# Performance work log

Hardware: AMD Instinct MI355X
Metric: run time of the kernel (lower is better)

## Reference

```python
import jax, jax.numpy as jnp
import numpy as np

N = 100000        # num nodes
F_IN = 256        # params['topo_feature']
C = 128           # params['num_edge'] (hidden & GCN channels)
E = 1_600_000     # num edges (avg degree 16)


def setup_inputs() -> dict:
    key = jax.random.key(0)
    k = jax.random.split(key, 6)
    x = jax.random.normal(k[0], (N, F_IN), dtype=jnp.float32)
    edge_index = jax.random.randint(k[1], (2, E), 0, N, dtype=jnp.int32)
    # fc1: Linear(F_IN, C)
    W1 = jax.random.normal(k[2], (C, F_IN), dtype=jnp.float32) * (1.0 / np.sqrt(F_IN))
    b1 = jnp.zeros((C,), dtype=jnp.float32)
    # GCNConv linear: Linear(C, C, bias=False) weight + separate bias added post-aggregation
    W2 = jax.random.normal(k[3], (C, C), dtype=jnp.float32) * (1.0 / np.sqrt(C))
    b2 = jnp.zeros((C,), dtype=jnp.float32)
    return {"x": x, "edge_index": edge_index, "W1": W1, "b1": b1, "W2": W2, "b2": b2}


def reference(x, edge_index, W1, b1, W2, b2):
    # fc1 + relu
    h = jax.nn.relu(x @ W1.T + b1)                       # [N, C]
    # GCNConv: transform, add self-loops, sym-normalize, scatter-add
    z = h @ W2.T                                         # [N, C]
    loop = jnp.arange(N, dtype=edge_index.dtype)
    src = jnp.concatenate([edge_index[0], loop])         # [E+N]
    dst = jnp.concatenate([edge_index[1], loop])         # [E+N]
    deg = jax.ops.segment_sum(jnp.ones_like(dst, jnp.float32), dst, num_segments=N)
    dinv = jnp.where(deg > 0, jax.lax.rsqrt(jnp.maximum(deg, 1.0)), 0.0)
    norm = (dinv[src] * dinv[dst])[:, None]              # [E+N, 1]
    out = jax.ops.segment_sum(z[src] * norm, dst, num_segments=N) + b2
    return out
```

## Files before the change

kernel.cpp:

```cpp
#include <hip/hip_runtime.h>

typedef unsigned short ushort;
typedef __bf16 bf16x8 __attribute__((ext_vector_type(8)));
typedef float f32x4 __attribute__((ext_vector_type(4)));

#define F_IN 256
#define CCH  128
#define BSH  7
#define BNODES 128
#define NBUCK_PAD 1024
#define CHUNK 8192

#define LDA 40
#define EPS 152

__device__ __forceinline__ ushort f2bf(float f) {
    union { float f; unsigned i; } u; u.f = f;
    unsigned r = u.i + 0x7fffu + ((u.i >> 16) & 1u);
    return (ushort)(r >> 16);
}
__device__ __forceinline__ float2 bf2f2(unsigned u) {
    union { unsigned i; float f; } lo, hi;
    lo.i = u << 16;
    hi.i = u & 0xffff0000u;
    return make_float2(lo.f, hi.f);
}

__global__ void cvt_w(const float* __restrict__ w, ushort* __restrict__ wb, int n) {
    int i = blockIdx.x * 256 + threadIdx.x;
    if (i < n) wb[i] = f2bf(w[i]);
}

template<int MODE>
__global__ __launch_bounds__(256)
void gemm_mfma(const void* __restrict__ Ain, const ushort* __restrict__ Wb,
               const float* __restrict__ bias, const float* __restrict__ dinv,
               ushort* __restrict__ Cout, int M, int K)
{
    __shared__ ushort smem[128 * EPS];
    ushort* As = smem;
    ushort* Bs = smem + 128 * LDA;
    const int tid = threadIdx.x;
    const int wave = tid >> 6, lane = tid & 63;
    const int wm = (wave & 1) * 64, wn = (wave >> 1) * 64;
    const int lr = lane & 15;
    const int lq = lane >> 4;
    const int m0 = blockIdx.x * 128;

    f32x4 acc[4][4] = {};

    for (int k0 = 0; k0 < K; k0 += 32) {
        if (MODE == 0) {
            const float* A = (const float*)Ain;
#pragma unroll
            for (int it = 0; it < 2; it++) {
                int flat = tid + it * 256;
                int row = flat >> 2, kq = (flat & 3) * 8;
                float4 a0 = make_float4(0.f, 0.f, 0.f, 0.f);
                float4 a1 = make_float4(0.f, 0.f, 0.f, 0.f);
                if (m0 + row < M) {
                    a0 = *(const float4*)&A[(long)(m0 + row) * K + k0 + kq];
                    a1 = *(const float4*)&A[(long)(m0 + row) * K + k0 + kq + 4];
                }
                ushort u[8] = { f2bf(a0.x), f2bf(a0.y), f2bf(a0.z), f2bf(a0.w),
                                f2bf(a1.x), f2bf(a1.y), f2bf(a1.z), f2bf(a1.w) };
                *(uint4*)&As[row * LDA + kq] = *(uint4*)u;
            }
        } else {
            const ushort* A = (const ushort*)Ain;
#pragma unroll
            for (int it = 0; it < 2; it++) {
                int flat = tid + it * 256;
                int row = flat >> 2, kq = (flat & 3) * 8;
                uint4 a = make_uint4(0u, 0u, 0u, 0u);
                if (m0 + row < M)
                    a = *(const uint4*)&A[(long)(m0 + row) * K + k0 + kq];
                *(uint4*)&As[row * LDA + kq] = a;
            }
        }
#pragma unroll
        for (int it = 0; it < 2; it++) {
            int flat = tid + it * 256;
            int row = flat >> 2, kq = (flat & 3) * 8;
            uint4 b = *(const uint4*)&Wb[(long)row * K + k0 + kq];
            *(uint4*)&Bs[row * LDA + kq] = b;
        }
        __syncthreads();

        bf16x8 af[4], bfr[4];
#pragma unroll
        for (int t4 = 0; t4 < 4; t4++) {
            af[t4]  = *(bf16x8*)&As[(wm + t4 * 16 + lr) * LDA + lq * 8];
            bfr[t4] = *(bf16x8*)&Bs[(wn + t4 * 16 + lr) * LDA + lq * 8];
        }
#pragma unroll
        for (int i = 0; i < 4; i++)
#pragma unroll
            for (int j = 0; j < 4; j++)
                acc[i][j] = __builtin_amdgcn_mfma_f32_16x16x32_bf16(af[i], bfr[j], acc[i][j], 0, 0, 0);
        __syncthreads();
    }

    if (MODE == 0) {
        float bv[4];
#pragma unroll
        for (int j = 0; j < 4; j++) bv[j] = bias[wn + j * 16 + lr];
#pragma unroll
        for (int i = 0; i < 4; i++)
#pragma unroll
            for (int r = 0; r < 4; r++) {
                int row = wm + i * 16 + lq * 4 + r;
#pragma unroll
                for (int j = 0; j < 4; j++) {
                    float v = fmaxf(acc[i][j][r] + bv[j], 0.f);
                    smem[row * EPS + wn + j * 16 + lr] = f2bf(v);
                }
            }
    } else {
#pragma unroll
        for (int i = 0; i < 4; i++)
#pragma unroll
            for (int r = 0; r < 4; r++) {
                int row = wm + i * 16 + lq * 4 + r;
                float di = (m0 + row < M) ? dinv[m0 + row] : 0.f;
#pragma unroll
                for (int j = 0; j < 4; j++)
                    smem[row * EPS + wn + j * 16 + lr] = f2bf(acc[i][j][r] * di);
            }
    }
    __syncthreads();
    {
        int colq = tid & 15, row0 = tid >> 4;
#pragma unroll
        for (int i = 0; i < 8; i++) {
            int row = row0 + i * 16;
            if (m0 + row < M)
                *(uint4*)&Cout[(long)(m0 + row) * CCH + colq * 8] =
                    *(uint4*)&smem[row * EPS + colq * 8];
        }
    }
}

__global__ void zero1024(int* g) { g[threadIdx.x] = 0; }

__global__ __launch_bounds__(256)
void hist_kernel(const int* __restrict__ dst, int* __restrict__ ghist, int E)
{
    __shared__ int h[NBUCK_PAD];
    int t = threadIdx.x;
    for (int i = t; i < NBUCK_PAD; i += 256) h[i] = 0;
    __syncthreads();
    int cb = blockIdx.x * CHUNK;
    int ce = min(cb + CHUNK, E);
    for (int e = cb + t; e < ce; e += 256)
        atomicAdd(&h[dst[e] >> BSH], 1);
    __syncthreads();
    for (int i = t; i < NBUCK_PAD; i += 256)
        if (h[i]) atomicAdd(&ghist[i], h[i]);
}

__global__ void scan1024(const int* __restrict__ ghist, int* __restrict__ base,
                         int* __restrict__ cursor)
{
    __shared__ int s[NBUCK_PAD];
    int t = threadIdx.x;
    int v = ghist[t];
    s[t] = v;
    __syncthreads();
    for (int off = 1; off < 1024; off <<= 1) {
        int x = (t >= off) ? s[t - off] : 0;
        __syncthreads();
        s[t] += x;
        __syncthreads();
    }
    int excl = s[t] - v;
    base[t] = excl;
    cursor[t] = excl;
    if (t == 1023) base[1024] = s[t];
}

__global__ __launch_bounds__(256)
void partition_kernel(const int* __restrict__ src, const int* __restrict__ dst,
                      int* __restrict__ cursor, unsigned* __restrict__ pairs, int E)
{
    __shared__ int lhist[NBUCK_PAD];
    __shared__ int lbase[NBUCK_PAD];
    __shared__ int rbase[NBUCK_PAD];
    __shared__ int ssum[256];
    __shared__ uint2 staged[CHUNK];
    int t = threadIdx.x;
    for (int i = t; i < NBUCK_PAD; i += 256) lhist[i] = 0;
    __syncthreads();
    int cb = blockIdx.x * CHUNK;
    int ce = min(cb + CHUNK, E);
    for (int e = cb + t; e < ce; e += 256)
        atomicAdd(&lhist[dst[e] >> BSH], 1);
    __syncthreads();
    int a0 = lhist[4 * t], a1 = lhist[4 * t + 1], a2 = lhist[4 * t + 2], a3 = lhist[4 * t + 3];
    int tsum = a0 + a1 + a2 + a3;
    ssum[t] = tsum;
    __syncthreads();
    for (int off = 1; off < 256; off <<= 1) {
        int x = (t >= off) ? ssum[t - off] : 0;
        __syncthreads();
        ssum[t] += x;
        __syncthreads();
    }
    int texcl = ssum[t] - tsum;
    lbase[4 * t]     = texcl;
    lbase[4 * t + 1] = texcl + a0;
    lbase[4 * t + 2] = texcl + a0 + a1;
    lbase[4 * t + 3] = texcl + a0 + a1 + a2;
    for (int i = t; i < NBUCK_PAD; i += 256) {
        int c = lhist[i];
        rbase[i] = c ? atomicAdd(&cursor[i], c) : 0;
        lhist[i] = 0;
    }
    __syncthreads();
    for (int e = cb + t; e < ce; e += 256) {
        int d = dst[e];
        int b = d >> BSH;
        unsigned packed = ((unsigned)src[e] << BSH) | (unsigned)(d & (BNODES - 1));
        int p = lbase[b] + atomicAdd(&lhist[b], 1);
        staged[p] = make_uint2(packed, (unsigned)b);
    }
    __syncthreads();
    int cnt = ce - cb;
    for (int i = t; i < cnt; i += 256) {
        uint2 sp = staged[i];
        int b = (int)sp.y;
        pairs[rbase[b] + (i - lbase[b])] = sp.x;
    }
}

__global__ __launch_bounds__(256)
void bucket_csr(const unsigned* __restrict__ pairs, const int* __restrict__ base,
                int* __restrict__ row_start, float* __restrict__ dinv,
                unsigned* __restrict__ csr, int N, int E)
{
    __shared__ int deg[BNODES];
    __shared__ int s[BNODES];
    __shared__ int cur[BNODES];
    const int b = blockIdx.x, t = threadIdx.x;
    if (t < BNODES) deg[t] = 0;
    __syncthreads();
    const int rb = base[b], re = base[b + 1];
    for (int e = rb + t; e < re; e += 256)
        atomicAdd(&deg[pairs[e] & (BNODES - 1)], 1);
    __syncthreads();
    int v = (t < BNODES) ? deg[t] : 0;
    if (t < BNODES) s[t] = v;
    __syncthreads();
    for (int off = 1; off < BNODES; off <<= 1) {
        int x = (t >= off && t < BNODES) ? s[t - off] : 0;
        __syncthreads();
        if (t < BNODES) s[t] += x;
        __syncthreads();
    }
    const int n0 = b << BSH;
    if (t < BNODES) {
        int excl = s[t] - v;
        cur[t] = excl;
        if (n0 + t < N) {
            row_start[n0 + t] = rb + excl;
            dinv[n0 + t] = rsqrtf((float)v + 1.0f);
        }
    }
    if (b == gridDim.x - 1 && t == 0) row_start[N] = E;
    __syncthreads();
    for (int e = rb + t; e < re; e += 256) {
        unsigned p = pairs[e];
        int l = p & (BNODES - 1);
        int slot = atomicAdd(&cur[l], 1);
        csr[rb + slot] = p >> BSH;
    }
}

__global__ __launch_bounds__(256)
void gather_nodes(const unsigned* __restrict__ zq, const unsigned* __restrict__ csr,
                  const int* __restrict__ row_start, const float* __restrict__ dinv,
                  const float* __restrict__ b2, float* __restrict__ out, int N)
{
    const int node = blockIdx.x * 4 + (threadIdx.x >> 6);
    const int lane = threadIdx.x & 63;
    if (node >= N) return;

    float2 zs = bf2f2(zq[(long)node * 64 + lane]);
    float acc0 = zs.x, acc1 = zs.y;

    const int rs = row_start[node];
    const int re = row_start[node + 1];
    int j = rs;
    for (; j + 8 <= re; j += 8) {
        unsigned sI[8], zv[8];
#pragma unroll
        for (int q = 0; q < 8; q++) sI[q] = csr[j + q];
#pragma unroll
        for (int q = 0; q < 8; q++) zv[q] = zq[(long)sI[q] * 64 + lane];
#pragma unroll
        for (int q = 0; q < 8; q++) { float2 f = bf2f2(zv[q]); acc0 += f.x; acc1 += f.y; }
    }
    for (; j < re; j++) {
        float2 f = bf2f2(zq[(long)csr[j] * 64 + lane]);
        acc0 += f.x; acc1 += f.y;
    }

    float di = dinv[node];
    float2 o;
    o.x = b2[lane * 2 + 0] + di * acc0;
    o.y = b2[lane * 2 + 1] + di * acc1;
    *(float2*)&out[(long)node * CCH + lane * 2] = o;
}

extern "C" void kernel_launch(void* const* d_in, const int* in_sizes, int n_in,
                              void* d_out, int out_size, void* d_ws, size_t ws_size,
                              hipStream_t stream)
{
    const float* x  = (const float*)d_in[0];
    const int*   ei = (const int*)d_in[1];
    const float* W1 = (const float*)d_in[2];
    const float* b1 = (const float*)d_in[3];
    const float* W2 = (const float*)d_in[4];
    const float* b2 = (const float*)d_in[5];
    float* out = (float*)d_out;

    const int N = in_sizes[0] / F_IN;
    const int E = in_sizes[1] / 2;
    const int* src = ei;
    const int* dst = ei + E;

    char* ws = (char*)d_ws;
    ushort* h     = (ushort*)ws;   ws += (size_t)N * CCH * 2;
    ushort* zq    = (ushort*)ws;   ws += (size_t)N * CCH * 2;
    ushort* w1b   = (ushort*)ws;   ws += (size_t)CCH * F_IN * 2;
    ushort* w2b   = (ushort*)ws;   ws += (size_t)CCH * CCH * 2;
    unsigned* prs = (unsigned*)ws; ws += (size_t)E * 4;
    unsigned* csr = (unsigned*)ws; ws += (size_t)E * 4;
    int* rstart   = (int*)ws;      ws += ((size_t)N + 1) * 4;
    float* dinv   = (float*)ws;    ws += (size_t)N * 4;
    int* ghist    = (int*)ws;      ws += NBUCK_PAD * 4;
    int* gbase    = (int*)ws;      ws += (NBUCK_PAD + 1) * 4;
    int* gcursor  = (int*)ws;      ws += NBUCK_PAD * 4;

    const int nchunks = (E + CHUNK - 1) / CHUNK;
    const int nbuck   = (N + BNODES - 1) / BNODES;
    const int ngrid   = (N + 127) / 128;

    zero1024<<<1, 1024, 0, stream>>>(ghist);
    hist_kernel<<<nchunks, 256, 0, stream>>>(dst, ghist, E);
    scan1024<<<1, 1024, 0, stream>>>(ghist, gbase, gcursor);
    partition_kernel<<<nchunks, 256, 0, stream>>>(src, dst, gcursor, prs, E);
    bucket_csr<<<nbuck, 256, 0, stream>>>(prs, gbase, rstart, dinv, csr, N, E);

    cvt_w<<<(CCH * F_IN + 255) / 256, 256, 0, stream>>>(W1, w1b, CCH * F_IN);
    cvt_w<<<(CCH * CCH + 255) / 256, 256, 0, stream>>>(W2, w2b, CCH * CCH);

    gemm_mfma<0><<<ngrid, 256, 0, stream>>>(x, w1b, b1, nullptr, h, N, F_IN);
    gemm_mfma<1><<<ngrid, 256, 0, stream>>>(h, w2b, nullptr, dinv, zq, N, CCH);

    gather_nodes<<<(N + 3) / 4, 256, 0, stream>>>((const unsigned*)zq, csr, rstart, dinv, b2, out, N);
}
```

Baseline: 355.7 us.

## Fuse both GEMMs and make edge partition deterministic via per-chunk histograms

Fuses the fc1 and GCN linear GEMMs into one kernel that keeps the ReLU'd hidden tile in shared memory, so the intermediate h never round-trips through global memory. The edge partition now writes per-chunk histograms, and a 2D scan turns them into fixed offsets. This replaces global atomic cursors and removes the histogram recomputation inside partition. Weight conversion is folded into the histogram kernel launch, which cuts the launch count. The trade-off is a serial per-bucket scan over all chunks in a single block, and more shared memory per GEMM block.

```diff
diff --git a/kernel.cpp b/kernel.cpp
--- a/kernel.cpp
+++ b/kernel.cpp
@@ -8,11 +8,11 @@
 #define CCH  128
 #define BSH  7
 #define BNODES 128
-#define NBUCK_PAD 1024
+#define NBUCK 1024
 #define CHUNK 8192
 
 #define LDA 40
-#define EPS 152
+#define LDH 136
 
 __device__ __forceinline__ ushort f2bf(float f) {
     union { float f; unsigned i; } u; u.f = f;
@@ -26,178 +26,72 @@
     return make_float2(lo.f, hi.f);
 }
 
-__global__ void cvt_w(const float* __restrict__ w, ushort* __restrict__ wb, int n) {
-    int i = blockIdx.x * 256 + threadIdx.x;
-    if (i < n) wb[i] = f2bf(w[i]);
-}
-
-template<int MODE>
-__global__ __launch_bounds__(256)
-void gemm_mfma(const void* __restrict__ Ain, const ushort* __restrict__ Wb,
-               const float* __restrict__ bias, const float* __restrict__ dinv,
-               ushort* __restrict__ Cout, int M, int K)
-{
-    __shared__ ushort smem[128 * EPS];
-    ushort* As = smem;
-    ushort* Bs = smem + 128 * LDA;
-    const int tid = threadIdx.x;
-    const int wave = tid >> 6, lane = tid & 63;
-    const int wm = (wave & 1) * 64, wn = (wave >> 1) * 64;
-    const int lr = lane & 15;
-    const int lq = lane >> 4;
-    const int m0 = blockIdx.x * 128;
-
-    f32x4 acc[4][4] = {};
-
-    for (int k0 = 0; k0 < K; k0 += 32) {
-        if (MODE == 0) {
-            const float* A = (const float*)Ain;
-#pragma unroll
-            for (int it = 0; it < 2; it++) {
-                int flat = tid + it * 256;
-                int row = flat >> 2, kq = (flat & 3) * 8;
-                float4 a0 = make_float4(0.f, 0.f, 0.f, 0.f);
-                float4 a1 = make_float4(0.f, 0.f, 0.f, 0.f);
-                if (m0 + row < M) {
-                    a0 = *(const float4*)&A[(long)(m0 + row) * K + k0 + kq];
-                    a1 = *(const float4*)&A[(long)(m0 + row) * K + k0 + kq + 4];
-                }
-                ushort u[8] = { f2bf(a0.x), f2bf(a0.y), f2bf(a0.z), f2bf(a0.w),
-                                f2bf(a1.x), f2bf(a1.y), f2bf(a1.z), f2bf(a1.w) };
-                *(uint4*)&As[row * LDA + kq] = *(uint4*)u;
-            }
-        } else {
-            const ushort* A = (const ushort*)Ain;
-#pragma unroll
-            for (int it = 0; it < 2; it++) {
-                int flat = tid + it * 256;
-                int row = flat >> 2, kq = (flat & 3) * 8;
-                uint4 a = make_uint4(0u, 0u, 0u, 0u);
-                if (m0 + row < M)
-                    a = *(const uint4*)&A[(long)(m0 + row) * K + k0 + kq];
-                *(uint4*)&As[row * LDA + kq] = a;
-            }
-        }
-#pragma unroll
-        for (int it = 0; it < 2; it++) {
-            int flat = tid + it * 256;
-            int row = flat >> 2, kq = (flat & 3) * 8;
-            uint4 b = *(const uint4*)&Wb[(long)row * K + k0 + kq];
-            *(uint4*)&Bs[row * LDA + kq] = b;
-        }
-        __syncthreads();
-
-        bf16x8 af[4], bfr[4];
-#pragma unroll
-        for (int t4 = 0; t4 < 4; t4++) {
-            af[t4]  = *(bf16x8*)&As[(wm + t4 * 16 + lr) * LDA + lq * 8];
-            bfr[t4] = *(bf16x8*)&Bs[(wn + t4 * 16 + lr) * LDA + lq * 8];
-        }
-#pragma unroll
-        for (int i = 0; i < 4; i++)
-#pragma unroll
-            for (int j = 0; j < 4; j++)
-                acc[i][j] = __builtin_amdgcn_mfma_f32_16x16x32_bf16(af[i], bfr[j], acc[i][j], 0, 0, 0);
-        __syncthreads();
-    }
-
-    if (MODE == 0) {
-        float bv[4];
-#pragma unroll
-        for (int j = 0; j < 4; j++) bv[j] = bias[wn + j * 16 + lr];
-#pragma unroll
-        for (int i = 0; i < 4; i++)
-#pragma unroll
-            for (int r = 0; r < 4; r++) {
-                int row = wm + i * 16 + lq * 4 + r;
-#pragma unroll
-                for (int j = 0; j < 4; j++) {
-                    float v = fmaxf(acc[i][j][r] + bv[j], 0.f);
-                    smem[row * EPS + wn + j * 16 + lr] = f2bf(v);
-                }
-            }
-    } else {
-#pragma unroll
-        for (int i = 0; i < 4; i++)
-#pragma unroll
-            for (int r = 0; r < 4; r++) {
-                int row = wm + i * 16 + lq * 4 + r;
-                float di = (m0 + row < M) ? dinv[m0 + row] : 0.f;
-#pragma unroll
-                for (int j = 0; j < 4; j++)
-                    smem[row * EPS + wn + j * 16 + lr] = f2bf(acc[i][j][r] * di);
-            }
-    }
-    __syncthreads();
-    {
-        int colq = tid & 15, row0 = tid >> 4;
-#pragma unroll
-        for (int i = 0; i < 8; i++) {
-            int row = row0 + i * 16;
-            if (m0 + row < M)
-                *(uint4*)&Cout[(long)(m0 + row) * CCH + colq * 8] =
-                    *(uint4*)&smem[row * EPS + colq * 8];
-        }
-    }
-}
-
-__global__ void zero1024(int* g) { g[threadIdx.x] = 0; }
-
-__global__ __launch_bounds__(256)
-void hist_kernel(const int* __restrict__ dst, int* __restrict__ ghist, int E)
-{
-    __shared__ int h[NBUCK_PAD];
-    int t = threadIdx.x;
-    for (int i = t; i < NBUCK_PAD; i += 256) h[i] = 0;
-    __syncthreads();
-    int cb = blockIdx.x * CHUNK;
-    int ce = min(cb + CHUNK, E);
+__global__ __launch_bounds__(256)
+void hist_cvt(const int* __restrict__ dst, int* __restrict__ hist2D, int E, int nchunks,
+              const float* __restrict__ W1, const float* __restrict__ W2,
+              ushort* __restrict__ w1b, ushort* __restrict__ w2b)
+{
+    const int blk = blockIdx.x, t = threadIdx.x;
+    if (blk >= nchunks) {
+        int i = (blk - nchunks) * 256 + t;
+        if (i < CCH * F_IN) w1b[i] = f2bf(W1[i]);
+        else {
+            int j = i - CCH * F_IN;
+            if (j < CCH * CCH) w2b[j] = f2bf(W2[j]);
+        }
+        return;
+    }
+    __shared__ int h[NBUCK];
+    for (int i = t; i < NBUCK; i += 256) h[i] = 0;
+    __syncthreads();
+    int cb = blk * CHUNK, ce = min(cb + CHUNK, E);
     for (int e = cb + t; e < ce; e += 256)
         atomicAdd(&h[dst[e] >> BSH], 1);
     __syncthreads();
-    for (int i = t; i < NBUCK_PAD; i += 256)
-        if (h[i]) atomicAdd(&ghist[i], h[i]);
-}
-
-__global__ void scan1024(const int* __restrict__ ghist, int* __restrict__ base,
-                         int* __restrict__ cursor)
-{
-    __shared__ int s[NBUCK_PAD];
-    int t = threadIdx.x;
-    int v = ghist[t];
-    s[t] = v;
-    __syncthreads();
-    for (int off = 1; off < 1024; off <<= 1) {
+    for (int i = t; i < NBUCK; i += 256)
+        hist2D[blk * NBUCK + i] = h[i];
+}
+
+__global__ __launch_bounds__(1024)
+void scan2d(const int* __restrict__ hist2D, int* __restrict__ pref2D,
+            int* __restrict__ base, int nchunks)
+{
+    __shared__ int s[NBUCK];
+    const int t = threadIdx.x;
+    int run = 0;
+#pragma unroll 4
+    for (int c = 0; c < nchunks; c++) {
+        int v = hist2D[c * NBUCK + t];
+        pref2D[c * NBUCK + t] = run;
+        run += v;
+    }
+    s[t] = run;
+    __syncthreads();
+    for (int off = 1; off < NBUCK; off <<= 1) {
         int x = (t >= off) ? s[t - off] : 0;
         __syncthreads();
         s[t] += x;
         __syncthreads();
     }
-    int excl = s[t] - v;
-    base[t] = excl;
-    cursor[t] = excl;
-    if (t == 1023) base[1024] = s[t];
+    base[t] = s[t] - run;
+    if (t == NBUCK - 1) base[NBUCK] = s[t];
 }
 
 __global__ __launch_bounds__(256)
 void partition_kernel(const int* __restrict__ src, const int* __restrict__ dst,
-                      int* __restrict__ cursor, unsigned* __restrict__ pairs, int E)
-{
-    __shared__ int lhist[NBUCK_PAD];
-    __shared__ int lbase[NBUCK_PAD];
-    __shared__ int rbase[NBUCK_PAD];
+                      const int* __restrict__ hist2D, const int* __restrict__ pref2D,
+                      const int* __restrict__ base, unsigned* __restrict__ pairs, int E)
+{
+    __shared__ int lbase[NBUCK];
+    __shared__ int lcur[NBUCK];
+    __shared__ int rb2[NBUCK];
     __shared__ int ssum[256];
-    __shared__ uint2 staged[CHUNK];
-    int t = threadIdx.x;
-    for (int i = t; i < NBUCK_PAD; i += 256) lhist[i] = 0;
-    __syncthreads();
-    int cb = blockIdx.x * CHUNK;
-    int ce = min(cb + CHUNK, E);
-    for (int e = cb + t; e < ce; e += 256)
-        atomicAdd(&lhist[dst[e] >> BSH], 1);
-    __syncthreads();
-    int a0 = lhist[4 * t], a1 = lhist[4 * t + 1], a2 = lhist[4 * t + 2], a3 = lhist[4 * t + 3];
-    int tsum = a0 + a1 + a2 + a3;
+    __shared__ unsigned sp[CHUNK];
+    __shared__ ushort  sb[CHUNK];
+    const int t = threadIdx.x, blk = blockIdx.x;
+
+    int4 cv = *(const int4*)&hist2D[blk * NBUCK + 4 * t];
+    int tsum = cv.x + cv.y + cv.z + cv.w;
     ssum[t] = tsum;
     __syncthreads();
     for (int off = 1; off < 256; off <<= 1) {
@@ -208,28 +102,31 @@
     }
     int texcl = ssum[t] - tsum;
     lbase[4 * t]     = texcl;
-    lbase[4 * t + 1] = texcl + a0;
-    lbase[4 * t + 2] = texcl + a0 + a1;
-    lbase[4 * t + 3] = texcl + a0 + a1 + a2;
-    for (int i = t; i < NBUCK_PAD; i += 256) {
-        int c = lhist[i];
-        rbase[i] = c ? atomicAdd(&cursor[i], c) : 0;
-        lhist[i] = 0;
-    }
-    __syncthreads();
+    lbase[4 * t + 1] = texcl + cv.x;
+    lbase[4 * t + 2] = texcl + cv.x + cv.y;
+    lbase[4 * t + 3] = texcl + cv.x + cv.y + cv.z;
+    lcur[4 * t]     = lbase[4 * t];
+    lcur[4 * t + 1] = lbase[4 * t + 1];
+    lcur[4 * t + 2] = lbase[4 * t + 2];
+    lcur[4 * t + 3] = lbase[4 * t + 3];
+    for (int i = t; i < NBUCK; i += 256)
+        rb2[i] = base[i] + pref2D[blk * NBUCK + i];
+    __syncthreads();
+
+    const int cb = blk * CHUNK, ce = min(cb + CHUNK, E);
     for (int e = cb + t; e < ce; e += 256) {
         int d = dst[e];
         int b = d >> BSH;
         unsigned packed = ((unsigned)src[e] << BSH) | (unsigned)(d & (BNODES - 1));
-        int p = lbase[b] + atomicAdd(&lhist[b], 1);
-        staged[p] = make_uint2(packed, (unsigned)b);
-    }
-    __syncthreads();
-    int cnt = ce - cb;
+        int p = atomicAdd(&lcur[b], 1);
+        sp[p] = packed;
+        sb[p] = (ushort)b;
+    }
+    __syncthreads();
+    const int cnt = ce - cb;
     for (int i = t; i < cnt; i += 256) {
-        uint2 sp = staged[i];
-        int b = (int)sp.y;
-        pairs[rbase[b] + (i - lbase[b])] = sp.x;
+        int b = sb[i];
+        pairs[rb2[b] + (i - lbase[b])] = sp[i];
     }
 }
 
@@ -277,6 +174,117 @@
 }
 
 __global__ __launch_bounds__(256)
+void gemm_fused(const float* __restrict__ X, const ushort* __restrict__ W1b,
+                const ushort* __restrict__ W2b, const float* __restrict__ b1,
+                const float* __restrict__ dinv, ushort* __restrict__ Zq, int M)
+{
+    __shared__ ushort As[128 * LDA];
+    __shared__ ushort Bs[128 * LDA];
+    __shared__ ushort Ht[128 * LDH];
+    const int tid = threadIdx.x;
+    const int wave = tid >> 6, lane = tid & 63;
+    const int wm = (wave & 1) * 64, wn = (wave >> 1) * 64;
+    const int lr = lane & 15, lq = lane >> 4;
+    const int m0 = blockIdx.x * 128;
+
+    f32x4 acc[4][4] = {};
+    for (int k0 = 0; k0 < F_IN; k0 += 32) {
+#pragma unroll
+        for (int it = 0; it < 2; it++) {
+            int flat = tid + it * 256;
+            int row = flat >> 2, kq = (flat & 3) * 8;
+            float4 a0 = make_float4(0.f, 0.f, 0.f, 0.f);
+            float4 a1 = make_float4(0.f, 0.f, 0.f, 0.f);
+            if (m0 + row < M) {
+                a0 = *(const float4*)&X[(long)(m0 + row) * F_IN + k0 + kq];
+                a1 = *(const float4*)&X[(long)(m0 + row) * F_IN + k0 + kq + 4];
+            }
+            ushort u[8] = { f2bf(a0.x), f2bf(a0.y), f2bf(a0.z), f2bf(a0.w),
+                            f2bf(a1.x), f2bf(a1.y), f2bf(a1.z), f2bf(a1.w) };
+            *(uint4*)&As[row * LDA + kq] = *(uint4*)u;
+        }
+#pragma unroll
+        for (int it = 0; it < 2; it++) {
+            int flat = tid + it * 256;
+            int row = flat >> 2, kq = (flat & 3) * 8;
+            *(uint4*)&Bs[row * LDA + kq] = *(const uint4*)&W1b[(long)row * F_IN + k0 + kq];
+        }
+        __syncthreads();
+        bf16x8 af[4], bfr[4];
+#pragma unroll
+        for (int t4 = 0; t4 < 4; t4++) {
+            af[t4]  = *(bf16x8*)&As[(wm + t4 * 16 + lr) * LDA + lq * 8];
+            bfr[t4] = *(bf16x8*)&Bs[(wn + t4 * 16 + lr) * LDA + lq * 8];
+        }
+#pragma unroll
+        for (int i = 0; i < 4; i++)
+#pragma unroll
+            for (int j = 0; j < 4; j++)
+                acc[i][j] = __builtin_amdgcn_mfma_f32_16x16x32_bf16(af[i], bfr[j], acc[i][j], 0, 0, 0);
+        __syncthreads();
+    }
+    {
+        float bv[4];
+#pragma unroll
+        for (int j = 0; j < 4; j++) bv[j] = b1[wn + j * 16 + lr];
+#pragma unroll
+        for (int i = 0; i < 4; i++)
+#pragma unroll
+            for (int r = 0; r < 4; r++) {
+                int row = wm + i * 16 + lq * 4 + r;
+#pragma unroll
+                for (int j = 0; j < 4; j++)
+                    Ht[row * LDH + wn + j * 16 + lr] = f2bf(fmaxf(acc[i][j][r] + bv[j], 0.f));
+            }
+    }
+    __syncthreads();
+
+    f32x4 acc2[4][4] = {};
+    for (int k0 = 0; k0 < CCH; k0 += 32) {
+#pragma unroll
+        for (int it = 0; it < 2; it++) {
+            int flat = tid + it * 256;
+            int row = flat >> 2, kq = (flat & 3) * 8;
+            *(uint4*)&Bs[row * LDA + kq] = *(const uint4*)&W2b[(long)row * CCH + k0 + kq];
+        }
+        __syncthreads();
+        bf16x8 af[4], bfr[4];
+#pragma unroll
+        for (int t4 = 0; t4 < 4; t4++) {
+            af[t4]  = *(bf16x8*)&Ht[(wm + t4 * 16 + lr) * LDH + k0 + lq * 8];
+            bfr[t4] = *(bf16x8*)&Bs[(wn + t4 * 16 + lr) * LDA + lq * 8];
+        }
+#pragma unroll
+        for (int i = 0; i < 4; i++)
+#pragma unroll
+            for (int j = 0; j < 4; j++)
+                acc2[i][j] = __builtin_amdgcn_mfma_f32_16x16x32_bf16(af[i], bfr[j], acc2[i][j], 0, 0, 0);
+        __syncthreads();
+    }
+#pragma unroll
+    for (int i = 0; i < 4; i++)
+#pragma unroll
+        for (int r = 0; r < 4; r++) {
+            int row = wm + i * 16 + lq * 4 + r;
+            float di = (m0 + row < M) ? dinv[m0 + row] : 0.f;
+#pragma unroll
+            for (int j = 0; j < 4; j++)
+                Ht[row * LDH + wn + j * 16 + lr] = f2bf(acc2[i][j][r] * di);
+        }
+    __syncthreads();
+    {
+        int colq = tid & 15, row0 = tid >> 4;
+#pragma unroll
+        for (int i = 0; i < 8; i++) {
+            int row = row0 + i * 16;
+            if (m0 + row < M)
+                *(uint4*)&Zq[(long)(m0 + row) * CCH + colq * 8] =
+                    *(uint4*)&Ht[row * LDH + colq * 8];
+        }
+    }
+}
+
+__global__ __launch_bounds__(256)
 void gather_nodes(const unsigned* __restrict__ zq, const unsigned* __restrict__ csr,
                   const int* __restrict__ row_start, const float* __restrict__ dinv,
                   const float* __restrict__ b2, float* __restrict__ out, int N)
@@ -329,8 +337,12 @@
     const int* src = ei;
     const int* dst = ei + E;
 
+    const int nchunks = (E + CHUNK - 1) / CHUNK;
+    const int nbuck   = (N + BNODES - 1) / BNODES;
+    const int ngrid   = (N + 127) / 128;
+    const int ncvt    = (CCH * F_IN + CCH * CCH + 255) / 256;
+
     char* ws = (char*)d_ws;
-    ushort* h     = (ushort*)ws;   ws += (size_t)N * CCH * 2;
     ushort* zq    = (ushort*)ws;   ws += (size_t)N * CCH * 2;
     ushort* w1b   = (ushort*)ws;   ws += (size_t)CCH * F_IN * 2;
     ushort* w2b   = (ushort*)ws;   ws += (size_t)CCH * CCH * 2;
@@ -338,25 +350,16 @@
     unsigned* csr = (unsigned*)ws; ws += (size_t)E * 4;
     int* rstart   = (int*)ws;      ws += ((size_t)N + 1) * 4;
     float* dinv   = (float*)ws;    ws += (size_t)N * 4;
-    int* ghist    = (int*)ws;      ws += NBUCK_PAD * 4;
-    int* gbase    = (int*)ws;      ws += (NBUCK_PAD + 1) * 4;
-    int* gcursor  = (int*)ws;      ws += NBUCK_PAD * 4;
-
-    const int nchunks = (E + CHUNK - 1) / CHUNK;
-    const int nbuck   = (N + BNODES - 1) / BNODES;
-    const int ngrid   = (N + 127) / 128;
-
-    zero1024<<<1, 1024, 0, stream>>>(ghist);
-    hist_kernel<<<nchunks, 256, 0, stream>>>(dst, ghist, E);
-    scan1024<<<1, 1024, 0, stream>>>(ghist, gbase, gcursor);
-    partition_kernel<<<nchunks, 256, 0, stream>>>(src, dst, gcursor, prs, E);
+    int* hist2D   = (int*)ws;      ws += (size_t)nchunks * NBUCK * 4;
+    int* pref2D   = (int*)ws;      ws += (size_t)nchunks * NBUCK * 4;
+    int* gbase    = (int*)ws;      ws += (NBUCK + 1) * 4;
+
+    hist_cvt<<<nchunks + ncvt, 256, 0, stream>>>(dst, hist2D, E, nchunks, W1, W2, w1b, w2b);
+    scan2d<<<1, 1024, 0, stream>>>(hist2D, pref2D, gbase, nchunks);
+    partition_kernel<<<nchunks, 256, 0, stream>>>(src, dst, hist2D, pref2D, gbase, prs, E);
     bucket_csr<<<nbuck, 256, 0, stream>>>(prs, gbase, rstart, dinv, csr, N, E);
 
-    cvt_w<<<(CCH * F_IN + 255) / 256, 256, 0, stream>>>(W1, w1b, CCH * F_IN);
-    cvt_w<<<(CCH * CCH + 255) / 256, 256, 0, stream>>>(W2, w2b, CCH * CCH);
-
-    gemm_mfma<0><<<ngrid, 256, 0, stream>>>(x, w1b, b1, nullptr, h, N, F_IN);
-    gemm_mfma<1><<<ngrid, 256, 0, stream>>>(h, w2b, nullptr, dinv, zq, N, CCH);
+    gemm_fused<<<ngrid, 256, 0, stream>>>(x, w1b, w2b, b1, dinv, zq, N);
 
     gather_nodes<<<(N + 3) / 4, 256, 0, stream>>>((const unsigned*)zq, csr, rstart, dinv, b2, out, N);
 }
```

After: 338.3 us. -4.9%, faster.
